# Kernel optimization log

Measured on AMD Instinct MI355X. Metric: run time of the kernel, lower is better.

The kernel has to match this reference:

```python
import jax, jax.numpy as jnp
import numpy as np

N = 100000   # nodes
E = 1600000  # edges (before self-loops)
IN, HID, OUT = 128, 128, 64


def setup_inputs() -> dict:
    key = jax.random.key(0)
    ks = jax.random.split(key, 10)
    x = jax.random.normal(ks[0], (N, IN), dtype=jnp.float32)
    edge_index = jax.random.randint(ks[1], (2, E), 0, N)
    edge_weight = jax.random.uniform(ks[2], (E,), dtype=jnp.float32)
    # glorot-style init for the three GCNConv linear layers (with bias, PyG default)
    W1 = jax.random.normal(ks[3], (IN, HID), dtype=jnp.float32) * (1.0 / np.sqrt(IN))
    b1 = jnp.zeros((HID,), dtype=jnp.float32)
    W2 = jax.random.normal(ks[4], (HID, HID), dtype=jnp.float32) * (1.0 / np.sqrt(HID))
    b2 = jnp.zeros((HID,), dtype=jnp.float32)
    W3 = jax.random.normal(ks[5], (HID, OUT), dtype=jnp.float32) * (1.0 / np.sqrt(HID))
    b3 = jnp.zeros((OUT,), dtype=jnp.float32)
    return {"x": x, "edge_index": edge_index, "edge_weight": edge_weight,
            "W1": W1, "b1": b1, "W2": W2, "b2": b2, "W3": W3, "b3": b3}


def _gcn_norm(edge_index, edge_weight, num_nodes):
    """Add self-loops (weight 1) and compute symmetric D^-1/2 A D^-1/2 norm."""
    loop = jnp.arange(num_nodes)
    row = jnp.concatenate([edge_index[0], loop])
    col = jnp.concatenate([edge_index[1], loop])
    ew = jnp.concatenate([edge_weight, jnp.ones((num_nodes,), edge_weight.dtype)])
    deg = jax.ops.segment_sum(ew, col, num_segments=num_nodes)
    dinv = jnp.where(deg > 0, jax.lax.rsqrt(jnp.where(deg > 0, deg, 1.0)), 0.0)
    norm = dinv[row] * ew * dinv[col]  # [E+N]
    return row, col, norm


def _gcn_conv(h, row, col, norm, W, b, num_nodes):
    h = h @ W                                   # [N, d_out] dense transform first
    msg = h[row] * norm[:, None]                # gather + scale  [E+N, d_out]
    out = jax.ops.segment_sum(msg, col, num_segments=num_nodes)  # scatter-add
    return out + b


def reference(x, edge_index, edge_weight, W1, b1, W2, b2, W3, b3):
    num_nodes = x.shape[0]
    row, col, norm = _gcn_norm(edge_index, edge_weight, num_nodes)
    h = jax.nn.relu(_gcn_conv(x, row, col, norm, W1, b1, num_nodes))
    # dropout is identity in eval mode
    h = jax.nn.relu(_gcn_conv(h, row, col, norm, W2, b2, num_nodes))
    return _gcn_conv(h, row, col, norm, W3, b3, num_nodes)
```

## Files before the change

kernel.cpp:

```cpp
#include <hip/hip_runtime.h>
#include <hip/hip_bf16.h>
#include <hip/hip_fp16.h>


#define K_DIM 128
#define EPB 8192

using h4 = __attribute__((ext_vector_type(4))) _Float16;
using h8 = __attribute__((ext_vector_type(8))) _Float16;
using f16x4 = h4;
using f16x8 = h8;
typedef float f32x4 __attribute__((ext_vector_type(4)));

__global__ __launch_bounds__(256) void mhist_kernel(const int* __restrict__ col,
                                                    int* __restrict__ Hm, int e, int nb) {
    __shared__ int lcnt[1024];
    int blk = blockIdx.x, t = threadIdx.x;
    for (int i = t; i < nb; i += 256) lcnt[i] = 0;
    __syncthreads();
    int base = blk * EPB, end = min(base + EPB, e);
    for (int i = base + t; i < end; i += 256) atomicAdd(&lcnt[col[i] >> 7], 1);
    __syncthreads();
    for (int i = t; i < nb; i += 256) Hm[(size_t)blk * nb + i] = lcnt[i];
}

__global__ __launch_bounds__(256) void colscan_kernel(int* __restrict__ Hm,
                                                      int* __restrict__ bcnt,
                                                      int nblk, int nb) {
    int t = blockIdx.x * 4 + (threadIdx.x >> 6);
    int lane = threadIdx.x & 63;
    if (t >= nb) return;
    int carry = 0;
    for (int c0 = 0; c0 < nblk; c0 += 64) {
        int b = c0 + lane;
        int x = (b < nblk) ? Hm[(size_t)b * nb + t] : 0;
        int v = x;
        #pragma unroll
        for (int d = 1; d < 64; d <<= 1) {
            int y = __shfl_up(v, d, 64);
            if (lane >= d) v += y;
        }
        if (b < nblk) Hm[(size_t)b * nb + t] = carry + v - x;
        carry += __shfl(v, 63, 64);
    }
    if (lane == 0) bcnt[t] = carry;
}

__global__ __launch_bounds__(1024) void bscan2_kernel(const int* __restrict__ bcnt,
                                                      int* __restrict__ bptr,
                                                      int* __restrict__ nodeptr,
                                                      int nb, int nN, int etot) {
    __shared__ int wsum[16];
    int t = threadIdx.x, lane = t & 63, wid = t >> 6;
    int x = (t < nb) ? bcnt[t] : 0;
    int v = x;
    #pragma unroll
    for (int d = 1; d < 64; d <<= 1) {
        int y = __shfl_up(v, d, 64);
        if (lane >= d) v += y;
    }
    if (lane == 63) wsum[wid] = v;
    __syncthreads();
    if (wid == 0) {
        int s = (lane < 16) ? wsum[lane] : 0;
        #pragma unroll
        for (int d = 1; d < 16; d <<= 1) {
            int y = __shfl_up(s, d, 64);
            if (lane >= d) s += y;
        }
        if (lane < 16) wsum[lane] = s;
    }
    __syncthreads();
    int woff = (wid > 0) ? wsum[wid - 1] : 0;
    if (t < nb) bptr[t] = v + woff - x;
    if (t == 0) { bptr[nb] = etot; nodeptr[nN] = etot; }
}

__global__ void addbase_kernel(int* __restrict__ Hm, const int* __restrict__ bptr,
                               int nblk, int nb) {
    int i = blockIdx.x * blockDim.x + threadIdx.x;
    if (i < nblk * nb) Hm[i] += bptr[i % nb];
}

__global__ __launch_bounds__(256) void mscatter_kernel(const int* __restrict__ row,
                                                       const int* __restrict__ col,
                                                       const float* __restrict__ ew,
                                                       const int* __restrict__ Hm,
                                                       int2* __restrict__ ebuf,
                                                       int e, int nb) {
    __shared__ int2 sbuf[EPB];
    __shared__ unsigned short sbkt[EPB];
    __shared__ int lcnt[1024], lbase[1024], lfill[1024], garr[1024];
    int blk = blockIdx.x, t = threadIdx.x, lane = t & 63, wid = t >> 6;
    int base = blk * EPB, end = min(base + EPB, e);
    int cnt = end - base;
    if (cnt <= 0) return;
    for (int i = t; i < nb; i += 256) { garr[i] = Hm[(size_t)blk * nb + i]; lcnt[i] = 0; }
    __syncthreads();
    for (int i = base + t; i < end; i += 256) atomicAdd(&lcnt[col[i] >> 7], 1);
    __syncthreads();
    if (wid == 0) {
        int carry = 0;
        for (int c0 = 0; c0 < nb; c0 += 64) {
            int idx = c0 + lane;
            int x = (idx < nb) ? lcnt[idx] : 0;
            int v = x;
            #pragma unroll
            for (int d = 1; d < 64; d <<= 1) {
                int y = __shfl_up(v, d, 64);
                if (lane >= d) v += y;
            }
            if (idx < nb) { lbase[idx] = carry + v - x; lfill[idx] = carry + v - x; }
            carry += __shfl(v, 63, 64);
        }
    }
    __syncthreads();
    for (int i = base + t; i < end; i += 256) {
        int c = col[i];
        int b = c >> 7;
        int p = atomicAdd(&lfill[b], 1);
        sbuf[p] = make_int2(row[i] | ((c & 127) << 20), __float_as_int(ew[i]));
        sbkt[p] = (unsigned short)b;
    }
    __syncthreads();
    for (int j = t; j < cnt; j += 256) {
        int b = sbkt[j];
        ebuf[garr[b] + (j - lbase[b])] = sbuf[j];
    }
}

__global__ __launch_bounds__(256) void bbuild_kernel(const int2* __restrict__ ebuf,
                                                     const int* __restrict__ bptr,
                                                     int2* __restrict__ csr,
                                                     int* __restrict__ ptr, int n) {
    __shared__ int cnt[128];
    __shared__ int fil[128];
    int b = blockIdx.x;
    int t = threadIdx.x;
    int s = bptr[b], e = bptr[b + 1];
    if (t < 128) cnt[t] = 0;
    __syncthreads();
    for (int k = s + t; k < e; k += 256) {
        int c = (ebuf[k].x >> 20) & 127;
        atomicAdd(&cnt[c], 1);
    }
    __syncthreads();
    if (t < 64) {
        int lane = t;
        int v0 = cnt[lane], v1 = cnt[lane + 64];
        int i0 = v0, i1 = v1;
        #pragma unroll
        for (int d = 1; d < 64; d <<= 1) {
            int y0 = __shfl_up(i0, d, 64);
            int y1 = __shfl_up(i1, d, 64);
            if (lane >= d) { i0 += y0; i1 += y1; }
        }
        int tot0 = __shfl(i0, 63, 64);
        int e0 = i0 - v0;
        int e1 = i1 - v1 + tot0;
        fil[lane] = e0; fil[lane + 64] = e1;
        int node0 = b * 128 + lane;
        int node1 = node0 + 64;
        if (node0 < n) ptr[node0] = s + e0;
        if (node1 < n) ptr[node1] = s + e1;
    }
    __syncthreads();
    for (int k = s + t; k < e; k += 256) {
        int2 v = ebuf[k];
        int c = (v.x >> 20) & 127;
        int p = atomicAdd(&fil[c], 1);
        csr[s + p] = make_int2(v.x & 0xFFFFF, v.y);
    }
}

__global__ __launch_bounds__(256) void sortdeg_kernel(int2* __restrict__ csr,
                                                      const int* __restrict__ ptr,
                                                      float* __restrict__ dinv, int n) {
    int node = blockIdx.x * 4 + (threadIdx.x >> 6);
    int lane = threadIdx.x & 63;
    if (node >= n) return;
    int s = ptr[node], e = ptr[node + 1];
    int len = e - s;
    if (len <= 64) {
        int mx = 0x7FFFFFFF;
        unsigned my = 0xFFFFFFFFu;
        if (lane < len) {
            int2 v = csr[s + lane];
            mx = v.x; my = (unsigned)v.y;
        }
        #pragma unroll
        for (int k = 2; k <= 64; k <<= 1) {
            #pragma unroll
            for (int j = k >> 1; j > 0; j >>= 1) {
                int ox = __shfl_xor(mx, j, 64);
                unsigned oy = (unsigned)__shfl_xor((int)my, j, 64);
                bool up = ((lane & k) == 0);
                bool lower = ((lane & j) == 0);
                bool keep_min = (up == lower);
                bool me_gt  = (mx > ox) || (mx == ox && my > oy);
                bool oth_gt = (ox > mx) || (ox == mx && oy > my);
                bool take = keep_min ? me_gt : oth_gt;
                if (take) { mx = ox; my = oy; }
            }
        }
        if (lane < len) csr[s + lane] = make_int2(mx, (int)my);
        float w = (lane < len) ? __uint_as_float(my) : 0.f;
        #pragma unroll
        for (int d = 32; d; d >>= 1) w += __shfl_xor(w, d, 64);
        if (lane == 0) dinv[node] = rsqrtf(1.0f + w);
    } else {
        if (lane == 0) {
            for (int k = s + 1; k < e; ++k) {
                int2 key = csr[k];
                int j = k - 1;
                while (j >= s) {
                    int2 cj = csr[j];
                    bool gt = (cj.x > key.x) ||
                              (cj.x == key.x && (unsigned)cj.y > (unsigned)key.y);
                    if (!gt) break;
                    csr[j + 1] = cj;
                    --j;
                }
                csr[j + 1] = key;
            }
            float sum = 1.0f;
            for (int k = s; k < e; ++k) sum += __int_as_float(csr[k].y);
            dinv[node] = rsqrtf(sum);
        }
    }
}

__global__ void wcast_kernel(const float* __restrict__ W, _Float16* __restrict__ Wt,
                             int douts) {
    int i = blockIdx.x * blockDim.x + threadIdx.x;
    if (i < 128 * douts) {
        int k = i / douts, c = i % douts;
        Wt[c * 128 + k] = (_Float16)W[i];
    }
}

template <int DOUT, bool FP16IN>
__global__ __launch_bounds__(256) void mgemm_kernel(const void* __restrict__ Ap,
                                                    const _Float16* __restrict__ Wt,
                                                    const float* __restrict__ dinv,
                                                    _Float16* __restrict__ Tout, int nrows) {
    constexpr int BM = 128;
    constexpr int NCB = DOUT / 16;
    __shared__ f16x8 Als[BM * 16];
    __shared__ f16x8 Wls[DOUT * 16];
    int t = threadIdx.x;
    int row0 = blockIdx.x * BM;

    const f16x8* Wt8 = (const f16x8*)Wt;
    for (int i = t; i < DOUT * 16; i += 256) {
        int r = i >> 4, s = i & 15;
        Wls[r * 16 + (s ^ (r & 7))] = Wt8[i];
    }
    if constexpr (FP16IN) {
        const f16x8* A8 = (const f16x8*)Ap;
        for (int i = t; i < BM * 16; i += 256) {
            int r = i >> 4, s = i & 15;
            f16x8 v = {};
            int gr = row0 + r;
            if (gr < nrows) v = A8[(size_t)gr * 16 + s];
            Als[r * 16 + (s ^ (r & 7))] = v;
        }
    } else {
        const float* A = (const float*)Ap;
        f16x4* Als4 = (f16x4*)Als;
        for (int i = t; i < BM * 32; i += 256) {
            int r = i >> 5, c4 = i & 31;
            float4 v = make_float4(0.f, 0.f, 0.f, 0.f);
            int gr = row0 + r;
            if (gr < nrows) v = ((const float4*)(A + (size_t)gr * 128))[c4];
            f16x4 h;
            h[0] = (_Float16)v.x; h[1] = (_Float16)v.y;
            h[2] = (_Float16)v.z; h[3] = (_Float16)v.w;
            Als4[r * 32 + (c4 ^ ((r & 7) << 1))] = h;
        }
    }
    __syncthreads();

    int w = t >> 6, l = t & 63;
    int lcol = l & 15, lk = l >> 4;
    int wr0 = w * 32;

    f16x8 af[2][4];
    #pragma unroll
    for (int rb = 0; rb < 2; ++rb) {
        int r = wr0 + rb * 16 + lcol;
        #pragma unroll
        for (int kc = 0; kc < 4; ++kc) {
            int s = kc * 4 + lk;
            af[rb][kc] = Als[r * 16 + (s ^ (r & 7))];
        }
    }

    f32x4 acc[2][NCB] = {};
    #pragma unroll
    for (int cb = 0; cb < NCB; ++cb) {
        int c = cb * 16 + lcol;
        f16x8 bf[4];
        #pragma unroll
        for (int kc = 0; kc < 4; ++kc) {
            int s = kc * 4 + lk;
            bf[kc] = Wls[c * 16 + (s ^ (c & 7))];
        }
        #pragma unroll
        for (int rb = 0; rb < 2; ++rb) {
            #pragma unroll
            for (int kc = 0; kc < 4; ++kc)
                acc[rb][cb] = __builtin_amdgcn_mfma_f32_16x16x32_f16(
                    af[rb][kc], bf[kc], acc[rb][cb], 0, 0, 0);
        }
    }

    #pragma unroll
    for (int rb = 0; rb < 2; ++rb) {
        #pragma unroll
        for (int reg = 0; reg < 4; ++reg) {
            int gr = row0 + wr0 + rb * 16 + lk * 4 + reg;
            if (gr >= nrows) continue;
            float di = dinv[gr];
            #pragma unroll
            for (int cb = 0; cb < NCB; ++cb) {
                int c = cb * 16 + lcol;
                Tout[(size_t)gr * DOUT + c] = (_Float16)(acc[rb][cb][reg] * di);
            }
        }
    }
}

__global__ __launch_bounds__(256) void agg128_kernel(const _Float16* __restrict__ T,
                                                     const int* __restrict__ ptr,
                                                     const int2* __restrict__ csr,
                                                     const float* __restrict__ dinv,
                                                     const float* __restrict__ bias,
                                                     _Float16* __restrict__ out, int n) {
    int node = blockIdx.x * 16 + (threadIdx.x >> 4);
    int g = threadIdx.x & 15;
    if (node >= n) return;
    int s = ptr[node], e = ptr[node + 1];
    float di = dinv[node];
    const h8* Tv = (const h8*)T;
    float acc[8] = {};
    int k = s;
    for (; k + 3 < e; k += 4) {
        int2 e0 = csr[k], e1 = csr[k + 1], e2 = csr[k + 2], e3 = csr[k + 3];
        h8 v0 = Tv[(size_t)e0.x * 16 + g];
        h8 v1 = Tv[(size_t)e1.x * 16 + g];
        h8 v2 = Tv[(size_t)e2.x * 16 + g];
        h8 v3 = Tv[(size_t)e3.x * 16 + g];
        float w0 = __int_as_float(e0.y), w1 = __int_as_float(e1.y);
        float w2 = __int_as_float(e2.y), w3 = __int_as_float(e3.y);
        #pragma unroll
        for (int j = 0; j < 8; ++j) acc[j] += w0 * (float)v0[j];
        #pragma unroll
        for (int j = 0; j < 8; ++j) acc[j] += w1 * (float)v1[j];
        #pragma unroll
        for (int j = 0; j < 8; ++j) acc[j] += w2 * (float)v2[j];
        #pragma unroll
        for (int j = 0; j < 8; ++j) acc[j] += w3 * (float)v3[j];
    }
    for (; k < e; ++k) {
        int2 e0 = csr[k];
        h8 v0 = Tv[(size_t)e0.x * 16 + g];
        float w0 = __int_as_float(e0.y);
        #pragma unroll
        for (int j = 0; j < 8; ++j) acc[j] += w0 * (float)v0[j];
    }
    h8 hs = Tv[(size_t)node * 16 + g];
    #pragma unroll
    for (int j = 0; j < 8; ++j) acc[j] += (float)hs[j];
    float4 b0 = ((const float4*)bias)[g * 2];
    float4 b1 = ((const float4*)bias)[g * 2 + 1];
    float bb[8] = {b0.x, b0.y, b0.z, b0.w, b1.x, b1.y, b1.z, b1.w};
    h8 o;
    #pragma unroll
    for (int j = 0; j < 8; ++j) {
        float v = di * acc[j] + bb[j];
        o[j] = (_Float16)fmaxf(v, 0.f);
    }
    ((h8*)out)[(size_t)node * 16 + g] = o;
}

__global__ __launch_bounds__(256) void agg64_kernel(const _Float16* __restrict__ T,
                                                    const int* __restrict__ ptr,
                                                    const int2* __restrict__ csr,
                                                    const float* __restrict__ dinv,
                                                    const float* __restrict__ bias,
                                                    float* __restrict__ out, int n) {
    int node = blockIdx.x * 32 + (threadIdx.x >> 3);
    int g = threadIdx.x & 7;
    if (node >= n) return;
    int s = ptr[node], e = ptr[node + 1];
    float di = dinv[node];
    const h8* Tv = (const h8*)T;
    float acc[8] = {};
    int k = s;
    for (; k + 3 < e; k += 4) {
        int2 e0 = csr[k], e1 = csr[k + 1], e2 = csr[k + 2], e3 = csr[k + 3];
        h8 v0 = Tv[(size_t)e0.x * 8 + g];
        h8 v1 = Tv[(size_t)e1.x * 8 + g];
        h8 v2 = Tv[(size_t)e2.x * 8 + g];
        h8 v3 = Tv[(size_t)e3.x * 8 + g];
        float w0 = __int_as_float(e0.y), w1 = __int_as_float(e1.y);
        float w2 = __int_as_float(e2.y), w3 = __int_as_float(e3.y);
        #pragma unroll
        for (int j = 0; j < 8; ++j) acc[j] += w0 * (float)v0[j];
        #pragma unroll
        for (int j = 0; j < 8; ++j) acc[j] += w1 * (float)v1[j];
        #pragma unroll
        for (int j = 0; j < 8; ++j) acc[j] += w2 * (float)v2[j];
        #pragma unroll
        for (int j = 0; j < 8; ++j) acc[j] += w3 * (float)v3[j];
    }
    for (; k < e; ++k) {
        int2 e0 = csr[k];
        h8 v0 = Tv[(size_t)e0.x * 8 + g];
        float w0 = __int_as_float(e0.y);
        #pragma unroll
        for (int j = 0; j < 8; ++j) acc[j] += w0 * (float)v0[j];
    }
    h8 hs = Tv[(size_t)node * 8 + g];
    #pragma unroll
    for (int j = 0; j < 8; ++j) acc[j] += (float)hs[j];
    float4 b0 = ((const float4*)bias)[g * 2];
    float4 b1 = ((const float4*)bias)[g * 2 + 1];
    float4 o0, o1;
    o0.x = di * acc[0] + b0.x; o0.y = di * acc[1] + b0.y;
    o0.z = di * acc[2] + b0.z; o0.w = di * acc[3] + b0.w;
    o1.x = di * acc[4] + b1.x; o1.y = di * acc[5] + b1.y;
    o1.z = di * acc[6] + b1.z; o1.w = di * acc[7] + b1.w;
    ((float4*)out)[(size_t)node * 16 + g * 2] = o0;
    ((float4*)out)[(size_t)node * 16 + g * 2 + 1] = o1;
}

extern "C" void kernel_launch(void* const* d_in, const int* in_sizes, int n_in,
                              void* d_out, int out_size, void* d_ws, size_t ws_size,
                              hipStream_t stream) {
    const float* x   = (const float*)d_in[0];
    const int* eidx  = (const int*)d_in[1];
    const float* ew  = (const float*)d_in[2];
    const float* W1  = (const float*)d_in[3];
    const float* b1  = (const float*)d_in[4];
    const float* W2  = (const float*)d_in[5];
    const float* b2  = (const float*)d_in[6];
    const float* W3  = (const float*)d_in[7];
    const float* b3  = (const float*)d_in[8];

    const int N = in_sizes[0] / K_DIM;
    const int E = in_sizes[2];
    const int* erow = eidx;
    const int* ecol = eidx + E;
    const int NB = (N + 127) / 128;
    const int NBLK = (E + EPB - 1) / EPB;

    size_t off = 0;
    auto carve = [&](size_t bytes) {
        char* p = (char*)d_ws + off;
        off += (bytes + 255) & ~(size_t)255;
        return (void*)p;
    };
    int*   Hm   = (int*)carve((size_t)NBLK * NB * 4);
    int*   bcnt = (int*)carve((size_t)NB * 4);
    int*   bptr = (int*)carve((size_t)(NB + 1) * 4);
    int*   ptr  = (int*)carve((size_t)(N + 1) * 4);
    float* dinv = (float*)carve((size_t)N * 4);
    int2*  csr  = (int2*)carve((size_t)E * 8);
    size_t ubytes = (size_t)E * 8;
    if ((size_t)N * 128 * 2 > ubytes) ubytes = (size_t)N * 128 * 2;
    void* uni = carve(ubytes);
    int2*     ebuf = (int2*)uni;
    _Float16* Tf   = (_Float16*)uni;
    _Float16* Hact = (_Float16*)carve((size_t)N * 128 * 2);
    _Float16* T3   = (_Float16*)carve((size_t)N * 64 * 2);
    _Float16* Wt1 = (_Float16*)carve(128 * 128 * 2);
    _Float16* Wt2 = (_Float16*)carve(128 * 128 * 2);
    _Float16* Wt3 = (_Float16*)carve(64 * 128 * 2);
    (void)ws_size;

    float* out = (float*)d_out;

    wcast_kernel<<<64, 256, 0, stream>>>(W1, Wt1, 128);
    wcast_kernel<<<64, 256, 0, stream>>>(W2, Wt2, 128);
    wcast_kernel<<<32, 256, 0, stream>>>(W3, Wt3, 64);

    mhist_kernel<<<NBLK, 256, 0, stream>>>(ecol, Hm, E, NB);
    colscan_kernel<<<(NB + 3) / 4, 256, 0, stream>>>(Hm, bcnt, NBLK, NB);
    bscan2_kernel<<<1, 1024, 0, stream>>>(bcnt, bptr, ptr, NB, N, E);
    addbase_kernel<<<(NBLK * NB + 255) / 256, 256, 0, stream>>>(Hm, bptr, NBLK, NB);
    mscatter_kernel<<<NBLK, 256, 0, stream>>>(erow, ecol, ew, Hm, ebuf, E, NB);
    bbuild_kernel<<<NB, 256, 0, stream>>>(ebuf, bptr, csr, ptr, N);
    sortdeg_kernel<<<(N + 3) / 4, 256, 0, stream>>>(csr, ptr, dinv, N);

    int gG = (N + 127) / 128;
    int gAgg16 = (N + 15) / 16;
    int gAgg32 = (N + 31) / 32;

    mgemm_kernel<128, false><<<gG, 256, 0, stream>>>(x, Wt1, dinv, Tf, N);
    agg128_kernel<<<gAgg16, 256, 0, stream>>>(Tf, ptr, csr, dinv, b1, Hact, N);
    mgemm_kernel<128, true><<<gG, 256, 0, stream>>>(Hact, Wt2, dinv, Tf, N);
    agg128_kernel<<<gAgg16, 256, 0, stream>>>(Tf, ptr, csr, dinv, b2, Hact, N);
    mgemm_kernel<64, true><<<gG, 256, 0, stream>>>(Hact, Wt3, dinv, T3, N);
    agg64_kernel<<<gAgg32, 256, 0, stream>>>(T3, ptr, csr, dinv, b3, out, N);
}
```

Before: 344.0 us.

## Fuse bucket CSR build with per-node sort and degree into one kernel

Merges the bucket build kernel and the per-node sort/degree kernel into a single kernel that stages each 128-node bucket's edges in shared memory, sorts each node's segment there, and writes the sorted CSR and dinv once. This removes one launch and a global round trip over the CSR array. If a bucket exceeds the shared capacity it falls back to sorting in global memory. EPB is also halved, which doubles the histogram/scatter block count. The 32KB shared buffer may reduce occupancy.

```diff
diff --git a/kernel.cpp b/kernel.cpp
--- a/kernel.cpp
+++ b/kernel.cpp
@@ -4,7 +4,8 @@
 
 
 #define K_DIM 128
-#define EPB 8192
+#define EPB 4096
+#define BCAP 4096
 
 using h4 = __attribute__((ext_vector_type(4))) _Float16;
 using h8 = __attribute__((ext_vector_type(8))) _Float16;
@@ -129,24 +130,21 @@
     }
 }
 
-__global__ __launch_bounds__(256) void bbuild_kernel(const int2* __restrict__ ebuf,
-                                                     const int* __restrict__ bptr,
-                                                     int2* __restrict__ csr,
-                                                     int* __restrict__ ptr, int n) {
-    __shared__ int cnt[128];
-    __shared__ int fil[128];
-    int b = blockIdx.x;
-    int t = threadIdx.x;
+__global__ __launch_bounds__(256) void bsort_kernel(const int2* __restrict__ ebuf,
+                                                    const int* __restrict__ bptr,
+                                                    int2* __restrict__ csr,
+                                                    int* __restrict__ ptr,
+                                                    float* __restrict__ dinv, int n) {
+    __shared__ int2 sb[BCAP];
+    __shared__ int cnt[128], fil[128], base[128];
+    int b = blockIdx.x, t = threadIdx.x, lane = t & 63, wid = t >> 6;
     int s = bptr[b], e = bptr[b + 1];
+    int m = e - s;
     if (t < 128) cnt[t] = 0;
     __syncthreads();
-    for (int k = s + t; k < e; k += 256) {
-        int c = (ebuf[k].x >> 20) & 127;
-        atomicAdd(&cnt[c], 1);
-    }
+    for (int k = s + t; k < e; k += 256) atomicAdd(&cnt[(ebuf[k].x >> 20) & 127], 1);
     __syncthreads();
     if (t < 64) {
-        int lane = t;
         int v0 = cnt[lane], v1 = cnt[lane + 64];
         int i0 = v0, i1 = v1;
         #pragma unroll
@@ -158,74 +156,103 @@
         int tot0 = __shfl(i0, 63, 64);
         int e0 = i0 - v0;
         int e1 = i1 - v1 + tot0;
-        fil[lane] = e0; fil[lane + 64] = e1;
-        int node0 = b * 128 + lane;
-        int node1 = node0 + 64;
+        base[lane] = e0; base[lane + 64] = e1;
+        fil[lane] = e0;  fil[lane + 64] = e1;
+        int node0 = b * 128 + lane, node1 = node0 + 64;
         if (node0 < n) ptr[node0] = s + e0;
         if (node1 < n) ptr[node1] = s + e1;
     }
     __syncthreads();
-    for (int k = s + t; k < e; k += 256) {
-        int2 v = ebuf[k];
-        int c = (v.x >> 20) & 127;
-        int p = atomicAdd(&fil[c], 1);
-        csr[s + p] = make_int2(v.x & 0xFFFFF, v.y);
-    }
-}
-
-__global__ __launch_bounds__(256) void sortdeg_kernel(int2* __restrict__ csr,
-                                                      const int* __restrict__ ptr,
-                                                      float* __restrict__ dinv, int n) {
-    int node = blockIdx.x * 4 + (threadIdx.x >> 6);
-    int lane = threadIdx.x & 63;
-    if (node >= n) return;
-    int s = ptr[node], e = ptr[node + 1];
-    int len = e - s;
-    if (len <= 64) {
-        int mx = 0x7FFFFFFF;
-        unsigned my = 0xFFFFFFFFu;
-        if (lane < len) {
-            int2 v = csr[s + lane];
-            mx = v.x; my = (unsigned)v.y;
-        }
-        #pragma unroll
-        for (int k = 2; k <= 64; k <<= 1) {
+
+    bool fits = (m <= BCAP);
+    if (fits) {
+        for (int k = s + t; k < e; k += 256) {
+            int2 v = ebuf[k];
+            int c = (v.x >> 20) & 127;
+            int p = atomicAdd(&fil[c], 1);
+            sb[p] = make_int2(v.x & 0xFFFFF, v.y);
+        }
+    } else {
+        for (int k = s + t; k < e; k += 256) {
+            int2 v = ebuf[k];
+            int c = (v.x >> 20) & 127;
+            int p = atomicAdd(&fil[c], 1);
+            csr[s + p] = make_int2(v.x & 0xFFFFF, v.y);
+        }
+    }
+    __syncthreads();
+
+    for (int ni = wid; ni < 128; ni += 4) {
+        int node = b * 128 + ni;
+        if (node >= n) continue;
+        int llen = cnt[ni], ls = base[ni];
+        if (llen <= 64) {
+            int mx = 0x7FFFFFFF;
+            unsigned my = 0xFFFFFFFFu;
+            if (lane < llen) {
+                int2 v = fits ? sb[ls + lane] : csr[s + ls + lane];
+                mx = v.x; my = (unsigned)v.y;
+            }
             #pragma unroll
-            for (int j = k >> 1; j > 0; j >>= 1) {
-                int ox = __shfl_xor(mx, j, 64);
-                unsigned oy = (unsigned)__shfl_xor((int)my, j, 64);
-                bool up = ((lane & k) == 0);
-                bool lower = ((lane & j) == 0);
-                bool keep_min = (up == lower);
-                bool me_gt  = (mx > ox) || (mx == ox && my > oy);
-                bool oth_gt = (ox > mx) || (ox == mx && oy > my);
-                bool take = keep_min ? me_gt : oth_gt;
-                if (take) { mx = ox; my = oy; }
+            for (int k = 2; k <= 64; k <<= 1) {
+                #pragma unroll
+                for (int j = k >> 1; j > 0; j >>= 1) {
+                    int ox = __shfl_xor(mx, j, 64);
+                    unsigned oy = (unsigned)__shfl_xor((int)my, j, 64);
+                    bool up = ((lane & k) == 0);
+                    bool lower = ((lane & j) == 0);
+                    bool keep_min = (up == lower);
+                    bool me_gt  = (mx > ox) || (mx == ox && my > oy);
+                    bool oth_gt = (ox > mx) || (ox == mx && oy > my);
+                    bool take = keep_min ? me_gt : oth_gt;
+                    if (take) { mx = ox; my = oy; }
+                }
             }
-        }
-        if (lane < len) csr[s + lane] = make_int2(mx, (int)my);
-        float w = (lane < len) ? __uint_as_float(my) : 0.f;
-        #pragma unroll
-        for (int d = 32; d; d >>= 1) w += __shfl_xor(w, d, 64);
-        if (lane == 0) dinv[node] = rsqrtf(1.0f + w);
-    } else {
-        if (lane == 0) {
-            for (int k = s + 1; k < e; ++k) {
-                int2 key = csr[k];
-                int j = k - 1;
-                while (j >= s) {
-                    int2 cj = csr[j];
-                    bool gt = (cj.x > key.x) ||
-                              (cj.x == key.x && (unsigned)cj.y > (unsigned)key.y);
-                    if (!gt) break;
-                    csr[j + 1] = cj;
-                    --j;
+            if (lane < llen) csr[s + ls + lane] = make_int2(mx, (int)my);
+            float w = (lane < llen) ? __uint_as_float(my) : 0.f;
+            #pragma unroll
+            for (int d = 32; d; d >>= 1) w += __shfl_xor(w, d, 64);
+            if (lane == 0) dinv[node] = rsqrtf(1.0f + w);
+        } else if (lane == 0) {
+            if (fits) {
+                for (int k = 1; k < llen; ++k) {
+                    int2 key = sb[ls + k];
+                    int j = k - 1;
+                    while (j >= 0) {
+                        int2 cj = sb[ls + j];
+                        bool gt = (cj.x > key.x) ||
+                                  (cj.x == key.x && (unsigned)cj.y > (unsigned)key.y);
+                        if (!gt) break;
+                        sb[ls + j + 1] = cj;
+                        --j;
+                    }
+                    sb[ls + j + 1] = key;
                 }
-                csr[j + 1] = key;
+                float sum = 1.0f;
+                for (int k = 0; k < llen; ++k) {
+                    csr[s + ls + k] = sb[ls + k];
+                    sum += __int_as_float(sb[ls + k].y);
+                }
+                dinv[node] = rsqrtf(sum);
+            } else {
+                int gs = s + ls;
+                for (int k = 1; k < llen; ++k) {
+                    int2 key = csr[gs + k];
+                    int j = k - 1;
+                    while (j >= 0) {
+                        int2 cj = csr[gs + j];
+                        bool gt = (cj.x > key.x) ||
+                                  (cj.x == key.x && (unsigned)cj.y > (unsigned)key.y);
+                        if (!gt) break;
+                        csr[gs + j + 1] = cj;
+                        --j;
+                    }
+                    csr[gs + j + 1] = key;
+                }
+                float sum = 1.0f;
+                for (int k = 0; k < llen; ++k) sum += __int_as_float(csr[gs + k].y);
+                dinv[node] = rsqrtf(sum);
             }
-            float sum = 1.0f;
-            for (int k = s; k < e; ++k) sum += __int_as_float(csr[k].y);
-            dinv[node] = rsqrtf(sum);
         }
     }
 }
@@ -491,8 +518,7 @@
     bscan2_kernel<<<1, 1024, 0, stream>>>(bcnt, bptr, ptr, NB, N, E);
     addbase_kernel<<<(NBLK * NB + 255) / 256, 256, 0, stream>>>(Hm, bptr, NBLK, NB);
     mscatter_kernel<<<NBLK, 256, 0, stream>>>(erow, ecol, ew, Hm, ebuf, E, NB);
-    bbuild_kernel<<<NB, 256, 0, stream>>>(ebuf, bptr, csr, ptr, N);
-    sortdeg_kernel<<<(N + 3) / 4, 256, 0, stream>>>(csr, ptr, dinv, N);
+    bsort_kernel<<<NB, 256, 0, stream>>>(ebuf, bptr, csr, ptr, dinv, N);
 
     int gG = (N + 127) / 128;
     int gAgg16 = (N + 15) / 16;
```

Result: slower. 359.4 us (+4.5%).
